# Performance work log

Measured on AMD Instinct MI355X. Metric: run time of the kernel, lower is better.

The kernel has to match this reference:

```python
import jax, jax.numpy as jnp
import numpy as np
from jax import lax

GRID_SIZE = 5
SPLINE_ORDER = 3
GRID_RANGE = (-1.0, 1.0)
# (cin, cout, kernel, stride, pad) per KAN conv layer
CONVS = [(3, 16, 7, 2, 3), (16, 32, 3, 2, 1), (32, 64, 3, 2, 1)]


def make_grid(in_features):
    # uniform extended knot grid: (in_features, grid_size + 2*order + 1)
    h = (GRID_RANGE[1] - GRID_RANGE[0]) / GRID_SIZE
    g = jnp.arange(-SPLINE_ORDER, GRID_SIZE + SPLINE_ORDER + 1, dtype=jnp.float32) * h + GRID_RANGE[0]
    return jnp.broadcast_to(g, (in_features, g.shape[0]))


def b_splines(x, grid):
    # x: (N, in)  ->  (N, in, grid_size + order) via Cox-de Boor recursion
    x = x[..., None]
    bases = ((x >= grid[:, :-1]) & (x < grid[:, 1:])).astype(x.dtype)
    for k in range(1, SPLINE_ORDER + 1):
        left = (x - grid[:, : -(k + 1)]) / (grid[:, k:-1] - grid[:, : -(k + 1)])
        right = (grid[:, k + 1:] - x) / (grid[:, k + 1:] - grid[:, 1:-k])
        bases = left * bases[..., :-1] + right * bases[..., 1:]
    return bases


def kan_linear(x, grid, base_w, spline_w, spline_scaler):
    # base path: silu(x) @ W_base^T ; spline path: B(x) contracted with scaled spline coeffs
    base = jax.nn.silu(x) @ base_w.T
    bsp = b_splines(x, grid)                      # (N, in, K)
    scaled = spline_w * spline_scaler[..., None]  # (out, in, K)
    spline = jnp.einsum('nik,oik->no', bsp, scaled)
    return base + spline


def max_pool_2x2(x):
    return lax.reduce_window(x, -jnp.inf, lax.max, (1, 1, 2, 2), (1, 1, 2, 2), 'VALID')


def setup_inputs() -> dict:
    key = jax.random.key(0)
    ks = jax.random.split(key, 16)
    inp = {'x': jax.random.uniform(ks[0], (8, 3, 224, 224), dtype=jnp.float32)}
    dims = [(16, 147), (32, 144), (64, 288)]
    i = 1
    for li, (out_f, in_f) in enumerate(dims):
        inp[f'bw{li}'] = jax.random.normal(ks[i], (out_f, in_f), jnp.float32) / np.sqrt(in_f); i += 1
        inp[f'sw{li}'] = jax.random.normal(ks[i], (out_f, in_f, GRID_SIZE + SPLINE_ORDER), jnp.float32) * 0.1; i += 1
        inp[f'sc{li}'] = 1.0 + 0.1 * jax.random.normal(ks[i], (out_f, in_f), jnp.float32); i += 1
    inp['bwc'] = jax.random.normal(ks[i], (200, 64), jnp.float32) / 8.0; i += 1
    inp['swc'] = jax.random.normal(ks[i], (200, 64, GRID_SIZE + SPLINE_ORDER), jnp.float32) * 0.1; i += 1
    inp['scc'] = 1.0 + 0.1 * jax.random.normal(ks[i], (200, 64), jnp.float32)
    return inp


def reference(x, bw0, sw0, sc0, bw1, sw1, sc1, bw2, sw2, sc2, bwc, swc, scc):
    params = [(bw0, sw0, sc0), (bw1, sw1, sc1), (bw2, sw2, sc2)]
    h = x
    for i, (cin, cout, k, s, p) in enumerate(CONVS):
        # unfold: (B, cin*k*k, Ho, Wo) with channel-major patch ordering (matches torch unfold)
        patches = lax.conv_general_dilated_patches(
            h, (k, k), (s, s), [(p, p), (p, p)],
            dimension_numbers=('NCHW', 'OIHW', 'NCHW'))
        B, F_, Ho, Wo = patches.shape
        flat = patches.transpose(0, 2, 3, 1).reshape(-1, F_)  # (B*Ho*Wo, cin*k*k)
        y = kan_linear(flat, make_grid(F_), *params[i])
        h = y.reshape(B, Ho, Wo, cout).transpose(0, 3, 1, 2)
        h = jax.nn.relu(h)
        if i < len(CONVS) - 1:
            h = max_pool_2x2(h)
    h = h.mean(axis=(2, 3))  # adaptive avg pool to 1x1 + flatten -> (B, 64)
    return kan_linear(h, make_grid(h.shape[1]), bwc, swc, scc)
```

## Files before the change

kernel.cpp:

```cpp
#include <hip/hip_runtime.h>

#define DEV __device__ __forceinline__

typedef _Float16 f16x8 __attribute__((ext_vector_type(8)));
typedef float f32x4 __attribute__((ext_vector_type(4)));
typedef unsigned int u32x4 __attribute__((ext_vector_type(4)));
typedef unsigned int u32x4a __attribute__((ext_vector_type(4), aligned(4)));

DEV f16x8 kan_feats8(float x) {
    const float sil = x / (1.0f + __expf(-x));
    const float k0 = (float)(-3) * 0.4f - 1.0f;
    const float t = (x - k0) * 2.5f;
    const float mf = floorf(t);
    const int m = (int)mf;
    const float u = t - mf, v = 1.0f - u;
    const float u2 = u * u, u3 = u2 * u;
    const float N0 = v * v * v * (1.0f / 6.0f);
    const float N1 = (3.0f * u3 - 6.0f * u2 + 4.0f) * (1.0f / 6.0f);
    const float N2 = (-3.0f * u3 + 3.0f * u2 + 3.0f * u + 1.0f) * (1.0f / 6.0f);
    const float N3 = u3 * (1.0f / 6.0f);
    f16x8 g;
    g[0] = (_Float16)sil;
#pragma unroll
    for (int jj = 0; jj < 6; ++jj) {
        const int j = jj + 2;
        float val = 0.0f;
        val = (m == j + 3) ? N0 : val;
        val = (m == j + 2) ? N1 : val;
        val = (m == j + 1) ? N2 : val;
        val = (m == j)     ? N3 : val;
        g[1 + jj] = (_Float16)val;
    }
    g[7] = (_Float16)0.0f;
    return g;
}

DEV void kan_feats9(float x, float* f) {
    f[0] = x / (1.0f + __expf(-x));
    const float k0 = (float)(-3) * 0.4f - 1.0f;
    const float t = (x - k0) * 2.5f;
    const float mf = floorf(t);
    const int m = (int)mf;
    const float u = t - mf, v = 1.0f - u;
    const float u2 = u * u, u3 = u2 * u;
    const float N0 = v * v * v * (1.0f / 6.0f);
    const float N1 = (3.0f * u3 - 6.0f * u2 + 4.0f) * (1.0f / 6.0f);
    const float N2 = (-3.0f * u3 + 3.0f * u2 + 3.0f * u + 1.0f) * (1.0f / 6.0f);
    const float N3 = u3 * (1.0f / 6.0f);
#pragma unroll
    for (int j = 0; j < 8; ++j) {
        float val = 0.0f;
        val = (m == j + 3) ? N0 : val;
        val = (m == j + 2) ? N1 : val;
        val = (m == j + 1) ? N2 : val;
        val = (m == j)     ? N3 : val;
        f[1 + j] = val;
    }
}

__device__ constexpr int d_l0(int ii) {
    const int i = ii > 146 ? 146 : ii;
    const int ci = i / 49, rem = i % 49, kh = rem / 7, kw = rem % 7;
    return ((((kw & 1) * 3 + ci) * 13 + kh) * 19 + (kw >> 1)) * 16;
}
__device__ constexpr int d_l1(int i) {
    const int ch = i / 9, rem = i % 9, kh = rem / 3, kw = rem % 3;
    return ((((kw & 1) * 16 + ch) * 9 + kh) * 5 + (kw >> 1)) * 16;
}

template <int OUT_F, int IN_F>
DEV void pack_oct8(int g, const float* bw, const float* sw, const float* sc,
                   _Float16* W2) {
    const int o = g % OUT_F, i = g / OUT_F;
    f16x8 v;
    if (i < IN_F) {
        const int wi = o * IN_F + i;
        const float s = sc[wi];
        v[0] = (_Float16)bw[wi];
#pragma unroll
        for (int t = 1; t <= 6; ++t) v[t] = (_Float16)(sw[wi * 8 + t + 1] * s);
        v[7] = (_Float16)0.0f;
    } else {
#pragma unroll
        for (int t = 0; t < 8; ++t) v[t] = (_Float16)0.0f;
    }
    *(f16x8*)(W2 + g * 8) = v;
}

#define PS0 2368
#define PS1 4608
#define PS2 18432
#define PS3 12800
#define PS4 25088
#define PSUM (PS0 + PS1 + PS2 + PS3 + PS4)

__global__ __launch_bounds__(256) void prep_k(
    const float* __restrict__ bw0, const float* __restrict__ sw0, const float* __restrict__ sc0,
    const float* __restrict__ bw1, const float* __restrict__ sw1, const float* __restrict__ sc1,
    const float* __restrict__ bw2, const float* __restrict__ sw2, const float* __restrict__ sc2,
    const float* __restrict__ bwc, const float* __restrict__ swc, const float* __restrict__ scc,
    _Float16* __restrict__ W2_0, _Float16* __restrict__ W2_1, _Float16* __restrict__ W2_2,
    float* __restrict__ wcT, float* __restrict__ h2) {
    const int e = blockIdx.x * 256 + threadIdx.x;
    if (e < PS0) {
        pack_oct8<16, 147>(e, bw0, sw0, sc0, W2_0);
    } else if (e < PS0 + PS1) {
        pack_oct8<32, 144>(e - PS0, bw1, sw1, sc1, W2_1);
    } else if (e < PS0 + PS1 + PS2) {
        pack_oct8<64, 288>(e - PS0 - PS1, bw2, sw2, sc2, W2_2);
    } else if (e < PS0 + PS1 + PS2 + PS3) {
        const int ee = e - PS0 - PS1 - PS2;
        const int o = ee / 64, i = ee - o * 64;
        const float s = scc[ee];
        wcT[(i * 9 + 0) * 200 + o] = bwc[ee];
#pragma unroll
        for (int t = 0; t < 8; ++t)
            wcT[(i * 9 + 1 + t) * 200 + o] = swc[ee * 8 + t] * s;
    } else if (e < PSUM) {
        h2[e - PS0 - PS1 - PS2 - PS3] = 0.0f;
    }
}

__global__ __launch_bounds__(256, 4) void conv0_k(
    const float* __restrict__ x, const _Float16* __restrict__ W2,
    float* __restrict__ p0) {
    __shared__ __align__(16) _Float16 feats[1482 * 8];
    __shared__ float pb[4 * 8 * 16];
    const int tid = threadIdx.x;
    const int vt = blockIdx.x;
    const int b = vt / 196;
    const int r0 = vt - b * 196;
    const int bh = r0 / 7, bw = r0 - (r0 / 7) * 7;
    const int ih0 = bh * 8 - 3, iw0 = bw * 32 - 3;
    for (int t = tid; t < 1482; t += 256) {
        const int iwh = t % 19;
        int r = t / 19;
        const int ihp = r % 13; r /= 13;
        const int ci = r % 3;
        const int par = r / 3;
        const int ih = ih0 + ihp, iw = iw0 + 2 * iwh + par;
        float xv = 0.0f;
        if (ih >= 0 && ih < 224 && iw >= 0 && iw < 224)
            xv = x[((b * 3 + ci) * 224 + ih) * 224 + iw];
        *(f16x8*)(feats + t * 8) = kan_feats8(xv);
    }
    __syncthreads();
    const int lane = tid & 63, mt = tid >> 6;
    const int l15 = lane & 15, q = lane >> 4;
    const bool q1 = q & 1, q2 = q & 2;
    const char* aBase = (const char*)feats + ((2 * mt) * 19 + l15) * 16;
    const f16x8* __restrict__ Wv = (const f16x8*)W2;
    f32x4 acc = {0.f, 0.f, 0.f, 0.f};
#pragma unroll
    for (int s = 0; s < 37; ++s) {
        const int o0 = d_l0(4 * s), o1 = d_l0(4 * s + 1);
        const int o2 = d_l0(4 * s + 2), o3 = d_l0(4 * s + 3);
        const int e01 = q1 ? o1 : o0;
        const int e23 = q1 ? o3 : o2;
        const int aoff = q2 ? e23 : e01;
        const f16x8 a = *(const f16x8*)(aBase + aoff);
        const f16x8 bf = Wv[(s * 4 + q) * 16 + l15];
        acc = __builtin_amdgcn_mfma_f32_16x16x32_f16(a, bf, acc, 0, 0, 0);
    }
    pb[(mt * 8 + 2 * q + 0) * 16 + l15] = fmaxf(fmaxf(acc[0], 0.f), fmaxf(acc[1], 0.f));
    pb[(mt * 8 + 2 * q + 1) * 16 + l15] = fmaxf(fmaxf(acc[2], 0.f), fmaxf(acc[3], 0.f));
    __syncthreads();
    const int pr = tid >> 7, o = (tid >> 3) & 15, wp = tid & 7;
    const float v = fmaxf(pb[((2 * pr) * 8 + wp) * 16 + o],
                          pb[((2 * pr + 1) * 8 + wp) * 16 + o]);
    p0[((b * 16 + o) * 56 + bh * 2 + pr) * 56 + bw * 8 + wp] = v;
}

__global__ __launch_bounds__(256, 4) void conv1_k(
    const float* __restrict__ p0, const _Float16* __restrict__ W2,
    unsigned int* __restrict__ featP1) {
    __shared__ __align__(16) _Float16 feats[1440 * 8];
    __shared__ float abuf[2 * 32 * 16];
    const int tid = threadIdx.x;
    const int vt = blockIdx.x;
    const int b = vt / 49;
    const int r0 = vt - b * 49;
    const int bh = r0 / 7, bw = r0 - (r0 / 7) * 7;
    const int ih0 = bh * 8 - 1, iw0 = bw * 8 - 1;
    for (int t = tid; t < 1296; t += 256) {
        const int iwp = t % 9;
        int r = t / 9;
        const int ihp = r % 9;
        const int ch = r / 9;
        const int ih = ih0 + ihp, iw = iw0 + iwp;
        float xv = 0.0f;
        if (ih >= 0 && ih < 56 && iw >= 0 && iw < 56)
            xv = p0[((b * 16 + ch) * 56 + ih) * 56 + iw];
        const int slot = (((iwp & 1) * 16 + ch) * 9 + ihp) * 5 + (iwp >> 1);
        *(f16x8*)(feats + slot * 8) = kan_feats8(xv);
    }
    __syncthreads();
    const int lane = tid & 63, w = tid >> 6;
    const int kc = w >> 1, ot = w & 1;
    const int l15 = lane & 15, q = lane >> 4;
    const bool q1 = q & 1, q2 = q & 2;
    const int mh = l15 >> 2, mw = l15 & 3;
    const int ocol = ot * 16 + l15;
    const char* aBase = (const char*)feats + ((2 * mh) * 5 + mw) * 16 + kc * 5760;
    const f16x8* __restrict__ Wv = (const f16x8*)W2;
    f32x4 acc = {0.f, 0.f, 0.f, 0.f};
#pragma unroll
    for (int s = 0; s < 18; ++s) {
        const int o0 = d_l1(4 * s), o1 = d_l1(4 * s + 1);
        const int o2 = d_l1(4 * s + 2), o3 = d_l1(4 * s + 3);
        const int e01 = q1 ? o1 : o0;
        const int e23 = q1 ? o3 : o2;
        const int aoff = q2 ? e23 : e01;
        const f16x8 a = *(const f16x8*)(aBase + aoff);
        const f16x8 bf = Wv[(kc * 72 + s * 4 + q) * 32 + ocol];
        acc = __builtin_amdgcn_mfma_f32_16x16x32_f16(a, bf, acc, 0, 0, 0);
    }
#pragma unroll
    for (int reg = 0; reg < 4; ++reg)
        abuf[(kc * 32 + ocol) * 16 + q * 4 + reg] = acc[reg];
    __syncthreads();
    if (tid < 128) {
        const int o = tid >> 2, pp = tid & 3;
        const int hp = pp >> 1, wp = pp & 1;
        float mx = -1e30f;
#pragma unroll
        for (int dh = 0; dh < 2; ++dh)
#pragma unroll
            for (int dw = 0; dw < 2; ++dw) {
                const int m = (2 * hp + dh) * 4 + 2 * wp + dw;
                const float s = abuf[(0 * 32 + o) * 16 + m] + abuf[(1 * 32 + o) * 16 + m];
                mx = fmaxf(mx, fmaxf(s, 0.0f));
            }
        const f16x8 g = kan_feats8(mx);
        const size_t idx = ((b * 32 + o) * 14 + bh * 2 + hp) * 14 + bw * 2 + wp;
        *(u32x4*)(featP1 + idx * 4) = __builtin_bit_cast(u32x4, g);
    }
}

__global__ __launch_bounds__(256, 4) void conv2_k(
    const unsigned int* __restrict__ fm, const _Float16* __restrict__ W2,
    float* __restrict__ h2) {
    __shared__ __align__(16) unsigned int featW[16 * 132];
    const int tid = threadIdx.x;
    const int task = blockIdx.x;
    const int ks = task % 3, rt = task / 3;
    const int lane = tid & 63, ot = tid >> 6;
    const int q = lane >> 4, l15 = lane & 15;
    const int ocol = ot * 16 + l15;
    const u32x4 F0p = __builtin_bit_cast(u32x4, kan_feats8(0.0f));
    const int i_in = tid & 31, rbase = tid >> 5;
    int hi0[2], wi0[2], pixb[2];
    bool rv[2];
#pragma unroll
    for (int t = 0; t < 2; ++t) {
        const int n = rt * 16 + rbase + t * 8;
        const int wo_ = n % 7, ho_ = (n / 7) % 7, b_ = n / 49;
        rv[t] = (n < 392);
        hi0[t] = ho_ * 2 - 1;
        wi0[t] = wo_ * 2 - 1;
        pixb[t] = b_ * 32 * 14 * 14;
    }
    f32x4 acc = {0.f, 0.f, 0.f, 0.f};
    const f16x8* __restrict__ Wv = (const f16x8*)W2;
    for (int c = ks * 3; c < ks * 3 + 3; ++c) {
        const int ii = c * 32 + i_in;
        const int ci = ii / 9, rem = ii - ci * 9;
        const int kh = rem / 3, kw = rem - kh * 3;
#pragma unroll
        for (int t = 0; t < 2; ++t) {
            const int hi = hi0[t] + kh, wi = wi0[t] + kw;
            const bool v = rv[t] && hi >= 0 && hi < 14 && wi >= 0 && wi < 14;
            u32x4 rec = F0p;
            if (v)
                rec = *(const u32x4*)(fm + (size_t)(pixb[t] + (ci * 14 + hi) * 14 + wi) * 4);
            *(u32x4*)(featW + (rbase + t * 8) * 132 + i_in * 4) = rec;
        }
        __syncthreads();
        const char* arow = (const char*)featW + l15 * 528 + q * 16;
#pragma unroll
        for (int s = 0; s < 8; ++s) {
            const f16x8 a = *(const f16x8*)(arow + s * 64);
            const f16x8 bf = Wv[(c * 32 + s * 4 + q) * 64 + ocol];
            acc = __builtin_amdgcn_mfma_f32_16x16x32_f16(a, bf, acc, 0, 0, 0);
        }
        __syncthreads();
    }
#pragma unroll
    for (int reg = 0; reg < 4; ++reg) {
        const int n = rt * 16 + q * 4 + reg;
        if (n < 392) {
            const int wo_ = n % 7, ho_ = (n / 7) % 7, b_ = n / 49;
            atomicAdd(h2 + ((b_ * 64 + ocol) * 7 + ho_) * 7 + wo_, acc[reg]);
        }
    }
}

__global__ __launch_bounds__(256) void head_k(
    const float* __restrict__ h2, const float* __restrict__ wT,
    float* __restrict__ out) {
    __shared__ float feat[64 * 9];
    const int n = blockIdx.x;
    const int tid = threadIdx.x;
    if (tid < 64) {
        const float* p = h2 + (n * 64 + tid) * 49;
        float s = 0.0f;
        for (int j = 0; j < 49; ++j) s += fmaxf(p[j], 0.0f);
        float f9[9];
        kan_feats9(s / 49.0f, f9);
#pragma unroll
        for (int t = 0; t < 9; ++t) feat[tid * 9 + t] = f9[t];
    }
    __syncthreads();
    for (int o = tid; o < 200; o += 256) {
        float sum = 0.0f;
        for (int j = 0; j < 576; ++j) sum += feat[j] * wT[j * 200 + o];
        out[n * 200 + o] = sum;
    }
}

extern "C" void kernel_launch(void* const* d_in, const int* in_sizes, int n_in,
                              void* d_out, int out_size, void* d_ws, size_t ws_size,
                              hipStream_t stream) {
    const float* x   = (const float*)d_in[0];
    const float* bw0 = (const float*)d_in[1];
    const float* sw0 = (const float*)d_in[2];
    const float* sc0 = (const float*)d_in[3];
    const float* bw1 = (const float*)d_in[4];
    const float* sw1 = (const float*)d_in[5];
    const float* sc1 = (const float*)d_in[6];
    const float* bw2 = (const float*)d_in[7];
    const float* sw2 = (const float*)d_in[8];
    const float* sc2 = (const float*)d_in[9];
    const float* bwc = (const float*)d_in[10];
    const float* swc = (const float*)d_in[11];
    const float* scc = (const float*)d_in[12];
    float* out = (float*)d_out;

    char* ws = (char*)d_ws;
    size_t off = 0;
    auto alloc = [&](size_t nbytes) {
        char* p = ws + off;
        off += (nbytes + 255) & ~(size_t)255;
        return p;
    };
    _Float16* W2_0 = (_Float16*)alloc(PS0 * 16);
    _Float16* W2_1 = (_Float16*)alloc(PS1 * 16);
    _Float16* W2_2 = (_Float16*)alloc(PS2 * 16);
    float* wcT = (float*)alloc(576 * 200 * 4);
    float* h2  = (float*)alloc(8 * 64 * 49 * 4);
    float* p0  = (float*)alloc((size_t)8 * 16 * 56 * 56 * 4);
    unsigned int* featP1 = (unsigned int*)alloc((size_t)8 * 32 * 14 * 14 * 16);

    prep_k<<<(PSUM + 255) / 256, 256, 0, stream>>>(
        bw0, sw0, sc0, bw1, sw1, sc1, bw2, sw2, sc2, bwc, swc, scc,
        W2_0, W2_1, W2_2, wcT, h2);
    conv0_k<<<1568, 256, 0, stream>>>(x, W2_0, p0);
    conv1_k<<<392, 256, 0, stream>>>(p0, W2_1, featP1);
    conv2_k<<<75, 256, 0, stream>>>(featP1, W2_2, h2);
    head_k<<<8, 256, 0, stream>>>(h2, wcT, out);
}
```

Before: 132.9 us.

## Fuse head into conv2 via last-block atomic counter; raise conv occupancy bounds

Removes the separate head kernel launch by having the last finishing conv2 block, found through an atomic counter reset in prep_k, run the pooling and classifier head for all 8 batch items. It also raises the launch-bounds occupancy hint for conv0 and conv1 from 4 to 5 waves per SIMD. This saves one launch gap, but the head now runs serially in a single block instead of 8 blocks, and the tighter register budget may cause spills.

```diff
diff --git a/kernel.cpp b/kernel.cpp
--- a/kernel.cpp
+++ b/kernel.cpp
@@ -5,7 +5,6 @@
 typedef _Float16 f16x8 __attribute__((ext_vector_type(8)));
 typedef float f32x4 __attribute__((ext_vector_type(4)));
 typedef unsigned int u32x4 __attribute__((ext_vector_type(4)));
-typedef unsigned int u32x4a __attribute__((ext_vector_type(4), aligned(4)));
 
 DEV f16x8 kan_feats8(float x) {
     const float sil = x / (1.0f + __expf(-x));
@@ -100,7 +99,7 @@
     const float* __restrict__ bw2, const float* __restrict__ sw2, const float* __restrict__ sc2,
     const float* __restrict__ bwc, const float* __restrict__ swc, const float* __restrict__ scc,
     _Float16* __restrict__ W2_0, _Float16* __restrict__ W2_1, _Float16* __restrict__ W2_2,
-    float* __restrict__ wcT, float* __restrict__ h2) {
+    float* __restrict__ wcT, float* __restrict__ h2, int* __restrict__ cnt) {
     const int e = blockIdx.x * 256 + threadIdx.x;
     if (e < PS0) {
         pack_oct8<16, 147>(e, bw0, sw0, sc0, W2_0);
@@ -118,10 +117,12 @@
             wcT[(i * 9 + 1 + t) * 200 + o] = swc[ee * 8 + t] * s;
     } else if (e < PSUM) {
         h2[e - PS0 - PS1 - PS2 - PS3] = 0.0f;
-    }
-}
-
-__global__ __launch_bounds__(256, 4) void conv0_k(
+    } else if (e == PSUM) {
+        *cnt = 0;
+    }
+}
+
+__global__ __launch_bounds__(256, 5) void conv0_k(
     const float* __restrict__ x, const _Float16* __restrict__ W2,
     float* __restrict__ p0) {
     __shared__ __align__(16) _Float16 feats[1482 * 8];
@@ -171,7 +172,7 @@
     p0[((b * 16 + o) * 56 + bh * 2 + pr) * 56 + bw * 8 + wp] = v;
 }
 
-__global__ __launch_bounds__(256, 4) void conv1_k(
+__global__ __launch_bounds__(256, 5) void conv1_k(
     const float* __restrict__ p0, const _Float16* __restrict__ W2,
     unsigned int* __restrict__ featP1) {
     __shared__ __align__(16) _Float16 feats[1440 * 8];
@@ -239,8 +240,10 @@
 
 __global__ __launch_bounds__(256, 4) void conv2_k(
     const unsigned int* __restrict__ fm, const _Float16* __restrict__ W2,
-    float* __restrict__ h2) {
+    float* __restrict__ h2, const float* __restrict__ wT,
+    float* __restrict__ out, int* __restrict__ cnt) {
     __shared__ __align__(16) unsigned int featW[16 * 132];
+    __shared__ int lastFlag;
     const int tid = threadIdx.x;
     const int task = blockIdx.x;
     const int ks = task % 3, rt = task / 3;
@@ -293,28 +296,32 @@
             atomicAdd(h2 + ((b_ * 64 + ocol) * 7 + ho_) * 7 + wo_, acc[reg]);
         }
     }
-}
-
-__global__ __launch_bounds__(256) void head_k(
-    const float* __restrict__ h2, const float* __restrict__ wT,
-    float* __restrict__ out) {
-    __shared__ float feat[64 * 9];
-    const int n = blockIdx.x;
-    const int tid = threadIdx.x;
-    if (tid < 64) {
-        const float* p = h2 + (n * 64 + tid) * 49;
-        float s = 0.0f;
-        for (int j = 0; j < 49; ++j) s += fmaxf(p[j], 0.0f);
-        float f9[9];
-        kan_feats9(s / 49.0f, f9);
-#pragma unroll
-        for (int t = 0; t < 9; ++t) feat[tid * 9 + t] = f9[t];
-    }
-    __syncthreads();
-    for (int o = tid; o < 200; o += 256) {
-        float sum = 0.0f;
-        for (int j = 0; j < 576; ++j) sum += feat[j] * wT[j * 200 + o];
-        out[n * 200 + o] = sum;
+    __syncthreads();
+    if (tid == 0) {
+        __threadfence();
+        lastFlag = (atomicAdd(cnt, 1) == 74);
+    }
+    __syncthreads();
+    if (!lastFlag) return;
+    __threadfence();
+    float* feat = (float*)featW;
+    for (int n = 0; n < 8; ++n) {
+        if (tid < 64) {
+            const float* p = h2 + (n * 64 + tid) * 49;
+            float s = 0.0f;
+            for (int j = 0; j < 49; ++j) s += fmaxf(p[j], 0.0f);
+            float f9[9];
+            kan_feats9(s / 49.0f, f9);
+#pragma unroll
+            for (int t = 0; t < 9; ++t) feat[tid * 9 + t] = f9[t];
+        }
+        __syncthreads();
+        for (int o = tid; o < 200; o += 256) {
+            float sum = 0.0f;
+            for (int j = 0; j < 576; ++j) sum += feat[j] * wT[j * 200 + o];
+            out[n * 200 + o] = sum;
+        }
+        __syncthreads();
     }
 }
 
@@ -348,14 +355,14 @@
     _Float16* W2_2 = (_Float16*)alloc(PS2 * 16);
     float* wcT = (float*)alloc(576 * 200 * 4);
     float* h2  = (float*)alloc(8 * 64 * 49 * 4);
+    int* cnt   = (int*)alloc(256);
     float* p0  = (float*)alloc((size_t)8 * 16 * 56 * 56 * 4);
     unsigned int* featP1 = (unsigned int*)alloc((size_t)8 * 32 * 14 * 14 * 16);
 
-    prep_k<<<(PSUM + 255) / 256, 256, 0, stream>>>(
+    prep_k<<<(PSUM + 256) / 256, 256, 0, stream>>>(
         bw0, sw0, sc0, bw1, sw1, sc1, bw2, sw2, sc2, bwc, swc, scc,
-        W2_0, W2_1, W2_2, wcT, h2);
+        W2_0, W2_1, W2_2, wcT, h2, cnt);
     conv0_k<<<1568, 256, 0, stream>>>(x, W2_0, p0);
     conv1_k<<<392, 256, 0, stream>>>(p0, W2_1, featP1);
-    conv2_k<<<75, 256, 0, stream>>>(featP1, W2_2, h2);
-    head_k<<<8, 256, 0, stream>>>(h2, wcT, out);
-}
+    conv2_k<<<75, 256, 0, stream>>>(featP1, W2_2, h2, wcT, out, cnt);
+}
```

Measured after the change: 200.5 us. 1.51x slower.
